# Optimization experiments

Hardware: AMD Instinct MI355X
Metric: run time of the kernel (lower is better)

## Reference

```python
import jax, jax.numpy as jnp
import numpy as np

N, DM, DE, DT, DEMB, H = 100000, 256, 172, 100, 256, 2
U, NB, K = 50000, 6000, 20
MSG = 2 * DM + DE + DT  # 784


def _t2v(t, w, b):
    # Time2Vec: cos(t * w + b) -> [..., DT]
    return jnp.cos(t[..., None] * w + b)


def _gru(x, h, w_ih, w_hh, b_ih, b_hh):
    gi = x @ w_ih.T + b_ih
    gh = h @ w_hh.T + b_hh
    ir, iz, inn = jnp.split(gi, 3, axis=-1)
    hr, hz, hn = jnp.split(gh, 3, axis=-1)
    r = jax.nn.sigmoid(ir + hr)
    z = jax.nn.sigmoid(iz + hz)
    n = jnp.tanh(inn + r * hn)
    return (1.0 - z) * n + z * h


def setup_inputs() -> dict:
    key = jax.random.key(0)
    ks = jax.random.split(key, 32)
    s = 0.02
    return {
        'memory': jax.random.normal(ks[0], (N, DM), jnp.float32),
        'last_update': jax.random.uniform(ks[1], (N,), jnp.float32),
        'unique_msg': jax.random.normal(ks[2], (U, MSG), jnp.float32),
        'times': jax.random.uniform(ks[3], (NB,), jnp.float32),
        'nbr_times': jax.random.uniform(ks[4], (NB, K), jnp.float32),
        'nbr_feats': jax.random.normal(ks[5], (NB, K, DE), jnp.float32),
        't2v_w': jax.random.normal(ks[6], (DT,), jnp.float32),
        't2v_b': jax.random.normal(ks[7], (DT,), jnp.float32),
        'gru_w_ih': jax.random.normal(ks[8], (3 * DM, MSG), jnp.float32) * s,
        'gru_w_hh': jax.random.normal(ks[9], (3 * DM, DM), jnp.float32) * s,
        'gru_b_ih': jnp.zeros((3 * DM,), jnp.float32),
        'gru_b_hh': jnp.zeros((3 * DM,), jnp.float32),
        'w_q': jax.random.normal(ks[10], (DEMB, DM + DT), jnp.float32) * s,
        'w_k': jax.random.normal(ks[11], (DEMB, DM + DE + DT), jnp.float32) * s,
        'w_v': jax.random.normal(ks[12], (DEMB, DM + DE + DT), jnp.float32) * s,
        'w_out': jax.random.normal(ks[13], (DEMB, DEMB + DM), jnp.float32) * s,
        'b_out': jnp.zeros((DEMB,), jnp.float32),
        'lp_src_w': jax.random.normal(ks[14], (DEMB, DEMB), jnp.float32) * s,
        'lp_src_b': jnp.zeros((DEMB,), jnp.float32),
        'lp_dst_w': jax.random.normal(ks[15], (DEMB, DEMB), jnp.float32) * s,
        'lp_dst_b': jnp.zeros((DEMB,), jnp.float32),
        'lp_out_w': jax.random.normal(ks[16], (1, DEMB), jnp.float32) * s,
        'lp_out_b': jnp.zeros((1,), jnp.float32),
        'unique_nids': jnp.arange(U, dtype=jnp.int32),
        'nids': jax.random.randint(ks[17], (NB,), 0, N, jnp.int32),
        'nbr_nids': jax.random.randint(ks[18], (NB, K), 0, N, jnp.int32),
        'nbr_mask': jnp.ones((NB, K), jnp.int32),
    }


def reference(memory, last_update, unique_msg, times, nbr_times, nbr_feats,
              t2v_w, t2v_b, gru_w_ih, gru_w_hh, gru_b_ih, gru_b_hh,
              w_q, w_k, w_v, w_out, b_out,
              lp_src_w, lp_src_b, lp_dst_w, lp_dst_b, lp_out_w, lp_out_b,
              unique_nids, nids, nbr_nids, nbr_mask):
    # --- GRU memory update on unique nodes (get_updated_memory) ---
    h_new = _gru(unique_msg, memory[unique_nids], gru_w_ih, gru_w_hh, gru_b_ih, gru_b_hh)
    mem = memory.at[unique_nids].set(h_new)  # [N, DM]

    # --- temporal deltas (batch.time -= last_update[node]) ---
    t_adj = times - last_update[nids]            # [NB]
    delta = nbr_times - t_adj[:, None]           # [NB, K]

    q_time = _t2v(jnp.zeros((NB,), memory.dtype), t2v_w, t2v_b)  # [NB, DT]
    nbr_time = _t2v(delta, t2v_w, t2v_b)                          # [NB, K, DT]

    node_feat = mem[nids]        # [NB, DM]
    nbr_node = mem[nbr_nids]     # [NB, K, DM]

    dh = DEMB // H
    q_in = jnp.concatenate([node_feat, q_time], axis=-1)               # [NB, DM+DT]
    k_in = jnp.concatenate([nbr_node, nbr_feats, nbr_time], axis=-1)   # [NB, K, DM+DE+DT]
    q = (q_in @ w_q.T).reshape(NB, H, dh)
    k = (k_in @ w_k.T).reshape(NB, K, H, dh)
    v = (k_in @ w_v.T).reshape(NB, K, H, dh)

    scores = jnp.einsum('nhd,nkhd->nhk', q, k) / jnp.sqrt(jnp.asarray(dh, q.dtype))
    scores = jnp.where(nbr_mask[:, None, :] > 0, scores, jnp.asarray(-1e9, scores.dtype))
    attn = jax.nn.softmax(scores, axis=-1)                              # [NB, H, K]
    attn_out = jnp.einsum('nhk,nkhd->nhd', attn, v).reshape(NB, DEMB)

    z = jax.nn.relu(jnp.concatenate([attn_out, node_feat], axis=-1) @ w_out.T + b_out)  # [NB, DEMB]
    z_src, z_dst, z_neg = jnp.split(z, 3, axis=0)

    def link_pred(a, b):
        hh = jax.nn.relu(a @ lp_src_w.T + lp_src_b + b @ lp_dst_w.T + lp_dst_b)
        return jax.nn.sigmoid(hh @ lp_out_w.T + lp_out_b).reshape(-1)

    pos_out = link_pred(z_src, z_dst)
    neg_out = link_pred(z_src, z_neg)
    return (pos_out, neg_out)
```

## Files before the change

kernel.cpp:

```cpp
#include <hip/hip_runtime.h>
#include <math.h>

constexpr int kN    = 100000;
constexpr int kDM   = 256;
constexpr int kDE   = 172;
constexpr int kDT   = 100;
constexpr int kDEMB = 256;
constexpr int kDH   = 128;
constexpr int kH    = 2;
constexpr int kU    = 50000;
constexpr int kNB   = 6000;
constexpr int kK    = 20;
constexpr int kMSG  = 784;
constexpr int kQIN  = kDM + kDT;
constexpr int kKIN  = kDM + kDE + kDT;
constexpr int kZIN  = kDEMB + kDM;
constexpr int kMPAD = 50048;
constexpr int kKP1  = 832;
constexpr int kGN   = 768;

constexpr int kNKROWS = kNB * kK;
constexpr int kNKPAD  = 120064;
constexpr int kF2V    = 320;
constexpr int kQINP   = 384;
constexpr int kNBPAD  = 6016;
constexpr int kKVLD   = kKIN + 48;

typedef __bf16 bf16x8 __attribute__((ext_vector_type(8)));
typedef float  f32x4  __attribute__((ext_vector_type(4)));

__device__ __forceinline__ float sigmoidf_(float x){ return 1.0f/(1.0f+expf(-x)); }

__device__ __forceinline__ unsigned short f2bf(float f){
  unsigned int u = __float_as_uint(f);
  unsigned int r = (u + 0x7FFFu + ((u >> 16) & 1u)) >> 16;
  return (unsigned short)r;
}
__device__ __forceinline__ float bf2f(unsigned short u){
  return __uint_as_float(((unsigned int)u) << 16);
}

__device__ __forceinline__ void cvt_group(const float* __restrict__ src,
    unsigned short* __restrict__ dst, int vrows, int vcols, int sld, int dld,
    int r, int c8)
{
  unsigned short o[8];
  if (r < vrows && c8 + 7 < vcols) {
    const float* s = src + (size_t)r * sld + c8;
    const float4 a = *(const float4*)s;
    const float4 b = *(const float4*)(s + 4);
    o[0]=f2bf(a.x); o[1]=f2bf(a.y); o[2]=f2bf(a.z); o[3]=f2bf(a.w);
    o[4]=f2bf(b.x); o[5]=f2bf(b.y); o[6]=f2bf(b.z); o[7]=f2bf(b.w);
  } else if (r < vrows && c8 < vcols) {
    #pragma unroll
    for (int q=0;q<8;q++){
      const int col = c8 + q;
      o[q] = (col < vcols) ? f2bf(src[(size_t)r*sld + col]) : (unsigned short)0;
    }
  } else {
    #pragma unroll
    for (int q=0;q<8;q++) o[q]=0;
  }
  *(uint4*)(dst + (size_t)r*dld + c8) = *(const uint4*)o;
}

__global__ __launch_bounds__(256) void cvt_big2(const float* __restrict__ mem,
    const float* __restrict__ umsg, unsigned short* __restrict__ memb,
    unsigned short* __restrict__ A1)
{
  constexpr int t1 = kN * 32;
  constexpr int t2 = kMPAD * 104;
  const int total = t1 + t2;
  for (int i = blockIdx.x*256 + threadIdx.x; i < total; i += gridDim.x*256) {
    if (i < t1) {
      const int r = i >> 5, c8 = (i & 31) << 3;
      cvt_group(mem, memb, kN, kDM, kDM, kDM, r, c8);
    } else {
      const int j = i - t1;
      const int r = j / 104, c8 = (j - r*104) << 3;
      cvt_group(umsg, A1, kU, kMSG, kMSG, kKP1, r, c8);
    }
  }
}

__global__ __launch_bounds__(256) void cvt_weights(
    const float* __restrict__ gw_ih, const float* __restrict__ gw_hh,
    const float* __restrict__ w_q, const float* __restrict__ w_k,
    const float* __restrict__ w_v, const float* __restrict__ w_out,
    const float* __restrict__ lp_sw, const float* __restrict__ lp_dw,
    unsigned short* __restrict__ W1b, unsigned short* __restrict__ W2b,
    unsigned short* __restrict__ wq_bf, unsigned short* __restrict__ wkv_bf,
    unsigned short* __restrict__ wo_bf, unsigned short* __restrict__ wlp_bf)
{
  constexpr int n0 = 768*104;
  constexpr int n1 = 768*32;
  constexpr int n2 = 256*48;
  constexpr int n3 = 256*72;
  constexpr int n4 = 256*72;
  constexpr int n5 = 256*64;
  constexpr int n6 = 256*32;
  constexpr int n7 = 256*32;
  constexpr int e0=n0, e1=e0+n1, e2=e1+n2, e3=e2+n3, e4=e3+n4, e5=e4+n5,
                e6=e5+n6, total=e6+n7;
  for (int i = blockIdx.x*256 + threadIdx.x; i < total; i += gridDim.x*256) {
    if (i < e0) {
      const int r = i/104, c8 = (i - r*104) << 3;
      cvt_group(gw_ih, W1b, kGN, kMSG, kMSG, kKP1, r, c8);
    } else if (i < e1) {
      const int j = i - e0, r = j >> 5, c8 = (j & 31) << 3;
      cvt_group(gw_hh, W2b, kGN, kDM, kDM, kDM, r, c8);
    } else if (i < e2) {
      const int j = i - e1, r = j/48, c8 = (j - r*48) << 3;
      cvt_group(w_q, wq_bf, kDEMB, kQIN, kQIN, kQINP, r, c8);
    } else if (i < e3) {
      const int j = i - e2, r = j/72, c8 = (j - r*72) << 3;
      cvt_group(w_k, wkv_bf, kDEMB, kKIN, kKIN, kKVLD, r, c8);
    } else if (i < e4) {
      const int j = i - e3, r = j/72, c8 = (j - r*72) << 3;
      cvt_group(w_v, wkv_bf + (size_t)kDEMB*kKVLD, kDEMB, kKIN, kKIN, kKVLD, r, c8);
    } else if (i < e5) {
      const int j = i - e4, r = j >> 6, c8 = (j & 63) << 3;
      cvt_group(w_out, wo_bf, kDEMB, kZIN, kZIN, kZIN, r, c8);
    } else if (i < e6) {
      const int j = i - e5, r = j >> 5, c8 = (j & 31) << 3;
      cvt_group(lp_sw, wlp_bf, kDEMB, kDEMB, kDEMB, kDEMB, r, c8);
    } else {
      const int j = i - e6, r = j >> 5, c8 = (j & 31) << 3;
      cvt_group(lp_dw, wlp_bf + kDEMB*kDEMB, kDEMB, kDEMB, kDEMB, kDEMB, r, c8);
    }
  }
}

template<int OUT_BF16, int RELU>
__global__ __launch_bounds__(256) void gemm_bt(
    const unsigned short* __restrict__ A0, int lda0,
    const int* __restrict__ aidx, int ksplit, int mvalid,
    const unsigned short* __restrict__ A1p, int lda1,
    const unsigned short* __restrict__ B, int ldb,
    void* __restrict__ Cv, const float* __restrict__ bias,
    int ktiles, int nblk, int ldc)
{
  __shared__ unsigned short smem[2*128*64];
  unsigned short* As = smem;
  unsigned short* Bs = smem + 128*64;
  __shared__ int idxs[128];

  const int t    = threadIdx.x;
  const int lane = t & 63;
  const int wid  = t >> 6;
  const int wr   = wid >> 1, wc = wid & 1;

  const int nwg = gridDim.x;
  const int q8  = nwg >> 3, r8 = nwg & 7;
  const int xcd = blockIdx.x & 7, off = blockIdx.x >> 3;
  const int w   = ((xcd < r8) ? xcd*(q8+1) : r8*(q8+1) + (xcd-r8)*q8) + off;
  const int mbase = (w / nblk) * 128;
  const int nbase = (w % nblk) * 128;

  if (aidx && t < 128) {
    const int mr = mbase + t;
    idxs[t] = (mr < mvalid) ? aidx[mr] : 0;
  }
  __syncthreads();

  f32x4 acc[4][4];
  #pragma unroll
  for (int mi=0;mi<4;mi++)
    #pragma unroll
    for (int ni=0;ni<4;ni++)
      acc[mi][ni] = (f32x4){0.f,0.f,0.f,0.f};

  const int lr = (lane & 15);
  const int lk = (lane >> 4) * 8;

  for (int kt = 0; kt < ktiles; ++kt) {
    const int k0 = kt * 64;
    #pragma unroll
    for (int it = 0; it < 4; ++it) {
      const int row = (t >> 3) + it * 32;
      const int col = (t & 7) * 8;
      const unsigned short* ga;
      if (kt < ksplit) {
        const int ridx = aidx ? idxs[row] : (mbase + row);
        ga = A0 + (size_t)ridx * lda0 + k0 + col;
      } else {
        ga = A1p + (size_t)(mbase + row) * lda1 + (k0 - ksplit*64) + col;
      }
      const unsigned short* gb = B + (size_t)(nbase + row) * ldb + k0 + col;
      char* la = (char*)As + it*4096 + t*16;
      char* lb = (char*)Bs + it*4096 + t*16;
      __builtin_amdgcn_global_load_lds(
          (const __attribute__((address_space(1))) void*)ga,
          (__attribute__((address_space(3))) void*)la, 16, 0, 0);
      __builtin_amdgcn_global_load_lds(
          (const __attribute__((address_space(1))) void*)gb,
          (__attribute__((address_space(3))) void*)lb, 16, 0, 0);
    }
    __syncthreads();

    #pragma unroll
    for (int kk = 0; kk < 64; kk += 32) {
      bf16x8 af[4], bf_[4];
      #pragma unroll
      for (int mi = 0; mi < 4; ++mi)
        af[mi] = *(const bf16x8*)(As + ((wr*64 + mi*16 + lr) * 64 + kk + lk));
      #pragma unroll
      for (int ni = 0; ni < 4; ++ni)
        bf_[ni] = *(const bf16x8*)(Bs + ((wc*64 + ni*16 + lr) * 64 + kk + lk));
      #pragma unroll
      for (int mi = 0; mi < 4; ++mi)
        #pragma unroll
        for (int ni = 0; ni < 4; ++ni)
          acc[mi][ni] = __builtin_amdgcn_mfma_f32_16x16x32_bf16(
              af[mi], bf_[ni], acc[mi][ni], 0, 0, 0);
    }
    __syncthreads();
  }

  if (OUT_BF16) {
    char* cbytes = (char*)smem;
    #pragma unroll
    for (int mi = 0; mi < 4; ++mi) {
      #pragma unroll
      for (int ni = 0; ni < 4; ++ni) {
        const int col_l = wc*64 + ni*16 + (lane & 15);
        const float bv = bias ? bias[nbase + col_l] : 0.f;
        #pragma unroll
        for (int r = 0; r < 4; ++r) {
          const int row_l = wr*64 + mi*16 + ((lane >> 4) << 2) + r;
          float v = acc[mi][ni][r] + bv;
          if (RELU) v = fmaxf(v, 0.f);
          const int byte = (row_l*256 + col_l*2) ^ ((row_l & 7) << 4);
          *(unsigned short*)(cbytes + byte) = f2bf(v);
        }
      }
    }
    __syncthreads();
    unsigned short* C = (unsigned short*)Cv;
    #pragma unroll
    for (int j = 0; j < 8; ++j) {
      const int idx = j*256 + t;
      const int row = idx >> 4;
      const int col = (idx & 15) * 8;
      const int byte = (row*256 + col*2) ^ ((row & 7) << 4);
      *(uint4*)(C + (size_t)(mbase + row)*ldc + nbase + col) =
          *(const uint4*)(cbytes + byte);
    }
  } else {
    #pragma unroll
    for (int mi = 0; mi < 4; ++mi) {
      #pragma unroll
      for (int ni = 0; ni < 4; ++ni) {
        const int col = nbase + wc*64 + ni*16 + (lane & 15);
        const float bv = bias ? bias[col] : 0.f;
        #pragma unroll
        for (int r = 0; r < 4; ++r) {
          const int row = mbase + wr*64 + mi*16 + ((lane >> 4) << 2) + r;
          float v = acc[mi][ni][r] + bv;
          if (RELU) v = fmaxf(v, 0.f);
          ((float*)Cv)[(size_t)row * ldc + col] = v;
        }
      }
    }
  }
}

__global__ __launch_bounds__(256) void gru_gate_bf(
    const unsigned short* __restrict__ Gi, const unsigned short* __restrict__ Gh,
    const float* __restrict__ memory, const float* __restrict__ b_ih,
    const float* __restrict__ b_hh, const int* __restrict__ unids,
    unsigned short* __restrict__ memb)
{
  const int r = blockIdx.x, j = threadIdx.x;
  const size_t gb = (size_t)r * kGN;
  const float ir  = bf2f(Gi[gb + j])       + b_ih[j];
  const float iz  = bf2f(Gi[gb + 256 + j]) + b_ih[256 + j];
  const float inn = bf2f(Gi[gb + 512 + j]) + b_ih[512 + j];
  const float hr  = bf2f(Gh[gb + j])       + b_hh[j];
  const float hz  = bf2f(Gh[gb + 256 + j]) + b_hh[256 + j];
  const float hn  = bf2f(Gh[gb + 512 + j]) + b_hh[512 + j];
  const int uid = unids[r];
  const float h = memory[(size_t)uid*kDM + j];
  const float rg = sigmoidf_(ir + hr);
  const float zg = sigmoidf_(iz + hz);
  const float ng = tanhf(inn + rg * hn);
  memb[(size_t)uid*kDM + j] = f2bf((1.f - zg) * ng + zg * h);
}

__global__ __launch_bounds__(256) void build_both(
    const float* __restrict__ nbr_feats, const float* __restrict__ nbr_times,
    const float* __restrict__ times, const float* __restrict__ last_upd,
    const int* __restrict__ nids,
    const float* __restrict__ t2v_w, const float* __restrict__ t2v_b,
    const unsigned short* __restrict__ memb,
    unsigned short* __restrict__ f2v, unsigned short* __restrict__ qin)
{
  constexpr int t1 = kNKPAD * 40;
  constexpr int t2 = kNBPAD * 48;
  const int total = t1 + t2;
  for (int i = blockIdx.x*256 + threadIdx.x; i < total; i += gridDim.x*256) {
    if (i < t1) {
      const int r  = i / 40;
      const int c8 = (i - r*40) << 3;
      unsigned short o[8];
      if (r >= kNKROWS || c8 >= 272) {
        #pragma unroll
        for (int q=0;q<8;q++) o[q]=0;
      } else if (c8 + 8 <= kDE - 4) {
        const float* s = nbr_feats + (size_t)r*kDE + c8;
        const float4 a = *(const float4*)s;
        const float4 b = *(const float4*)(s + 4);
        o[0]=f2bf(a.x); o[1]=f2bf(a.y); o[2]=f2bf(a.z); o[3]=f2bf(a.w);
        o[4]=f2bf(b.x); o[5]=f2bf(b.y); o[6]=f2bf(b.z); o[7]=f2bf(b.w);
      } else {
        const int n = r / kK;
        const float dlt = nbr_times[r] - (times[n] - last_upd[nids[n]]);
        #pragma unroll
        for (int q=0;q<8;q++){
          const int c = c8 + q;
          float v;
          if (c < kDE)       v = nbr_feats[(size_t)r*kDE + c];
          else if (c < 272)  { const int d = c - kDE; v = cosf(dlt*t2v_w[d] + t2v_b[d]); }
          else               v = 0.f;
          o[q] = f2bf(v);
        }
      }
      *(uint4*)(f2v + (size_t)r*kF2V + c8) = *(const uint4*)o;
    } else {
      const int j  = i - t1;
      const int r  = j / 48;
      const int c8 = (j - r*48) << 3;
      uint4 pack;
      if (r >= kNB) {
        pack = (uint4){0,0,0,0};
      } else if (c8 + 8 <= kDM) {
        pack = *(const uint4*)(memb + (size_t)nids[r]*kDM + c8);
      } else {
        unsigned short o[8];
        #pragma unroll
        for (int q=0;q<8;q++){
          const int c = c8 + q;
          float v = 0.f;
          if (c >= kDM && c < kQIN) v = cosf(t2v_b[c - kDM]);
          o[q] = f2bf(v);
        }
        pack = *(const uint4*)o;
      }
      *(uint4*)(qin + (size_t)r*kQINP + c8) = pack;
    }
  }
}

__global__ __launch_bounds__(256) void attn2_kernel(
    const float* __restrict__ qv, const unsigned short* __restrict__ kvf,
    const unsigned short* __restrict__ qin, const int* __restrict__ nbr_mask,
    unsigned short* __restrict__ aonf)
{
  __shared__ unsigned short kv[kK][kZIN];
  __shared__ float qv_s[kDEMB];
  __shared__ float red[kH*kK];
  __shared__ float attnw[kH][kK];

  const int n = blockIdx.x;
  const int t = threadIdx.x;

  qv_s[t] = qv[(size_t)n*kDEMB + t];
  {
    const uint4* src = (const uint4*)(kvf + (size_t)n*kK*kZIN);
    uint4* dst = (uint4*)(&kv[0][0]);
    #pragma unroll
    for (int i = 0; i < 5; ++i) dst[t + i*256] = src[t + i*256];
  }
  __syncthreads();

  {
    const int w = t >> 6, lane = t & 63;
    #pragma unroll
    for (int i = 0; i < 10; ++i) {
      const int p = w*10 + i;
      const int h = p / kK, k = p - (p/kK)*kK;
      const int base = h*kDH;
      float s = qv_s[base+lane]*bf2f(kv[k][base+lane])
              + qv_s[base+64+lane]*bf2f(kv[k][base+64+lane]);
      #pragma unroll
      for (int off=32; off; off>>=1) s += __shfl_xor(s, off, 64);
      if (lane == 0) {
        s *= 0.08838834764831845f;
        red[p] = (nbr_mask[(size_t)n*kK + k] > 0) ? s : -1e9f;
      }
    }
  }
  __syncthreads();

  if (t < kH) {
    float m = -1e30f;
    for (int k=0;k<kK;k++) m = fmaxf(m, red[t*kK+k]);
    float e[kK]; float ssum = 0.f;
    for (int k=0;k<kK;k++){ e[k] = expf(red[t*kK+k]-m); ssum += e[k]; }
    const float inv = 1.f/ssum;
    for (int k=0;k<kK;k++) attnw[t][k] = e[k]*inv;
  }
  __syncthreads();

  {
    const int h = t >> 7;
    float acc = 0.f;
    #pragma unroll
    for (int k=0;k<kK;k++) acc += attnw[h][k]*bf2f(kv[k][kDEMB + t]);
    aonf[(size_t)n*kZIN + t] = f2bf(acc);
    aonf[(size_t)n*kZIN + kDEMB + t] = qin[(size_t)n*kQINP + t];
  }
}

__global__ __launch_bounds__(256) void lp_small(
    const float* __restrict__ P, const float* __restrict__ spb,
    const float* __restrict__ dpb, const float* __restrict__ opw,
    const float* __restrict__ opb, float* __restrict__ out)
{
  __shared__ float wsum[4];
  const int b = blockIdx.x;
  const int neg = b / 2000;
  const int i = b - neg*2000;
  const int t = threadIdx.x;
  const int oth = 2000 + neg*2000 + i;
  float h = P[(size_t)i*kZIN + t] + spb[t] + P[(size_t)oth*kZIN + kDEMB + t] + dpb[t];
  float p = fmaxf(h, 0.f) * opw[t];
  #pragma unroll
  for (int off=32; off; off>>=1) p += __shfl_xor(p, off, 64);
  if ((t & 63) == 0) wsum[t>>6] = p;
  __syncthreads();
  if (t == 0)
    out[b] = sigmoidf_(wsum[0]+wsum[1]+wsum[2]+wsum[3] + opb[0]);
}

extern "C" void kernel_launch(void* const* d_in, const int* in_sizes, int n_in,
                              void* d_out, int out_size, void* d_ws, size_t ws_size,
                              hipStream_t stream)
{
  const float* memory   = (const float*)d_in[0];
  const float* last_upd = (const float*)d_in[1];
  const float* umsg     = (const float*)d_in[2];
  const float* times    = (const float*)d_in[3];
  const float* nbr_t    = (const float*)d_in[4];
  const float* nbr_f    = (const float*)d_in[5];
  const float* t2v_w    = (const float*)d_in[6];
  const float* t2v_b    = (const float*)d_in[7];
  const float* gw_ih    = (const float*)d_in[8];
  const float* gw_hh    = (const float*)d_in[9];
  const float* gb_ih    = (const float*)d_in[10];
  const float* gb_hh    = (const float*)d_in[11];
  const float* w_q      = (const float*)d_in[12];
  const float* w_k      = (const float*)d_in[13];
  const float* w_v      = (const float*)d_in[14];
  const float* w_out    = (const float*)d_in[15];
  const float* b_out    = (const float*)d_in[16];
  const float* lp_sw    = (const float*)d_in[17];
  const float* lp_sb    = (const float*)d_in[18];
  const float* lp_dw    = (const float*)d_in[19];
  const float* lp_db    = (const float*)d_in[20];
  const float* lp_ow    = (const float*)d_in[21];
  const float* lp_ob    = (const float*)d_in[22];
  const int*   unids    = (const int*)d_in[23];
  const int*   nids     = (const int*)d_in[24];
  const int*   nbrn     = (const int*)d_in[25];
  const int*   nbrm     = (const int*)d_in[26];

  char* ws = (char*)d_ws;
  unsigned short* memb    = (unsigned short*)ws;
  unsigned short* f2v     = (unsigned short*)(ws + 51200000);
  unsigned short* A1      = (unsigned short*)(ws + 128040960);
  unsigned short* W1b     = (unsigned short*)(ws + 211320832);
  unsigned short* W2b     = (unsigned short*)(ws + 212598784);
  unsigned short* Gi_bf   = (unsigned short*)(ws + 212992000);
  unsigned short* Gh_bf   = (unsigned short*)(ws + 289865728);
  unsigned short* kvf_bf  = (unsigned short*)(ws + 366739456);
  unsigned short* qin_bf  = (unsigned short*)(ws + 489684992);
  float*          qv_f    = (float*)(ws + 494305280);
  unsigned short* wq_bf   = (unsigned short*)(ws + 500465664);
  unsigned short* wkv_bf  = (unsigned short*)(ws + 500662272);
  unsigned short* aonf_bf = (unsigned short*)(ws + 501252096);
  unsigned short* wo_bf   = (unsigned short*)(ws + 507412480);
  unsigned short* z_bf    = (unsigned short*)(ws + 507674624);
  unsigned short* wlp_bf  = (unsigned short*)(ws + 510754816);
  float*          P_f     = (float*)(ws + 511016960);
  cvt_big2<<<2048, 256, 0, stream>>>(memory, umsg, memb, A1);
  cvt_weights<<<728, 256, 0, stream>>>(gw_ih, gw_hh, w_q, w_k, w_v, w_out,
                                       lp_sw, lp_dw,
                                       W1b, W2b, wq_bf, wkv_bf, wo_bf, wlp_bf);

  gemm_bt<1,0><<<(kMPAD/128)*6, 256, 0, stream>>>(
      A1, kKP1, nullptr, 13, kMPAD, A1, kKP1, W1b, kKP1,
      Gi_bf, nullptr, 13, 6, kGN);
  gemm_bt<1,0><<<(kMPAD/128)*6, 256, 0, stream>>>(
      memb, kDM, unids, 4, kU, memb, kDM, W2b, kDM,
      Gh_bf, nullptr, 4, 6, kGN);
  gru_gate_bf<<<kU, 256, 0, stream>>>(Gi_bf, Gh_bf, memory, gb_ih, gb_hh,
                                      unids, memb);

  build_both<<<4096, 256, 0, stream>>>(nbr_f, nbr_t, times, last_upd, nids,
                                       t2v_w, t2v_b, memb, f2v, qin_bf);

  gemm_bt<0,0><<<(kNBPAD/128)*2, 256, 0, stream>>>(
      qin_bf, kQINP, nullptr, 6, kNBPAD, qin_bf, kQINP, wq_bf, kQINP,
      qv_f, nullptr, 6, 2, kDEMB);
  gemm_bt<1,0><<<(kNKPAD/128)*4, 256, 0, stream>>>(
      memb, kDM, nbrn, 4, kNKROWS, f2v, kF2V, wkv_bf, kKVLD,
      kvf_bf, nullptr, 9, 4, kZIN);
  attn2_kernel<<<kNB, 256, 0, stream>>>(qv_f, kvf_bf, qin_bf, nbrm, aonf_bf);
  gemm_bt<1,1><<<(kNBPAD/128)*2, 256, 0, stream>>>(
      aonf_bf, kZIN, nullptr, 8, kNBPAD, aonf_bf, kZIN, wo_bf, kZIN,
      z_bf, b_out, 8, 2, kDEMB);
  gemm_bt<0,0><<<(kNBPAD/128)*4, 256, 0, stream>>>(
      z_bf, kDEMB, nullptr, 4, kNBPAD, z_bf, kDEMB, wlp_bf, kDEMB,
      P_f, nullptr, 4, 4, kZIN);
  lp_small<<<4000, 256, 0, stream>>>(P_f, lp_sb, lp_db, lp_ow, lp_ob,
                                     (float*)d_out);
}
```

Baseline: 576.2 us.

## Double-buffer LDS tiles in bf16 GEMM to overlap loads with MFMA

Doubles the shared-memory staging area in the bf16 GEMM and prefetches the next K tile with global_load_lds while MFMAs run on the current one. The gather row indices are also hoisted out of the K loop into registers. This aims to hide global-memory latency behind compute. The cost is twice the LDS per block, which may lower occupancy, and correctness relies on the end-of-iteration barrier waiting for the async loads to finish.

```diff
diff --git a/kernel.cpp b/kernel.cpp
--- a/kernel.cpp
+++ b/kernel.cpp
@@ -140,10 +140,9 @@
     void* __restrict__ Cv, const float* __restrict__ bias,
     int ktiles, int nblk, int ldc)
 {
-  __shared__ unsigned short smem[2*128*64];
-  unsigned short* As = smem;
-  unsigned short* Bs = smem + 128*64;
+  __shared__ unsigned short smem[4*128*64];
   __shared__ int idxs[128];
+  constexpr int kBuf = 2*128*64;
 
   const int t    = threadIdx.x;
   const int lane = t & 63;
@@ -163,6 +162,13 @@
   }
   __syncthreads();
 
+  const int srow = t >> 3;
+  const int scol = (t & 7) * 8;
+  int arow[4];
+  #pragma unroll
+  for (int it = 0; it < 4; ++it)
+    arow[it] = aidx ? idxs[srow + it*32] : (mbase + srow + it*32);
+
   f32x4 acc[4][4];
   #pragma unroll
   for (int mi=0;mi<4;mi++)
@@ -173,31 +179,35 @@
   const int lr = (lane & 15);
   const int lk = (lane >> 4) * 8;
 
-  for (int kt = 0; kt < ktiles; ++kt) {
+  auto stg = [&](int kt, int b){
     const int k0 = kt * 64;
+    char* la = (char*)(smem + b*kBuf);
+    char* lb = (char*)(smem + b*kBuf + 128*64);
     #pragma unroll
     for (int it = 0; it < 4; ++it) {
-      const int row = (t >> 3) + it * 32;
-      const int col = (t & 7) * 8;
       const unsigned short* ga;
-      if (kt < ksplit) {
-        const int ridx = aidx ? idxs[row] : (mbase + row);
-        ga = A0 + (size_t)ridx * lda0 + k0 + col;
-      } else {
-        ga = A1p + (size_t)(mbase + row) * lda1 + (k0 - ksplit*64) + col;
-      }
-      const unsigned short* gb = B + (size_t)(nbase + row) * ldb + k0 + col;
-      char* la = (char*)As + it*4096 + t*16;
-      char* lb = (char*)Bs + it*4096 + t*16;
+      if (kt < ksplit)
+        ga = A0 + (size_t)arow[it] * lda0 + k0 + scol;
+      else
+        ga = A1p + (size_t)(mbase + srow + it*32) * lda1 + (k0 - ksplit*64) + scol;
+      const unsigned short* gb = B + (size_t)(nbase + srow + it*32) * ldb + k0 + scol;
       __builtin_amdgcn_global_load_lds(
           (const __attribute__((address_space(1))) void*)ga,
-          (__attribute__((address_space(3))) void*)la, 16, 0, 0);
+          (__attribute__((address_space(3))) void*)(la + it*4096 + t*16), 16, 0, 0);
       __builtin_amdgcn_global_load_lds(
           (const __attribute__((address_space(1))) void*)gb,
-          (__attribute__((address_space(3))) void*)lb, 16, 0, 0);
-    }
-    __syncthreads();
-
+          (__attribute__((address_space(3))) void*)(lb + it*4096 + t*16), 16, 0, 0);
+    }
+  };
+
+  stg(0, 0);
+  __syncthreads();
+
+  for (int kt = 0; kt < ktiles; ++kt) {
+    const int cur = kt & 1;
+    if (kt + 1 < ktiles) stg(kt + 1, cur ^ 1);
+    const unsigned short* As = smem + cur*kBuf;
+    const unsigned short* Bs = As + 128*64;
     #pragma unroll
     for (int kk = 0; kk < 64; kk += 32) {
       bf16x8 af[4], bf_[4];
```

Measured after the change: 631.1 us. 9.5% more time.
